# Optimization experiments

Measured on AMD Instinct MI355X. Metric: run time of the kernel, lower is better.

Reference implementation:

```python
import jax, jax.numpy as jnp
import numpy as np

N, F, U, H = 4096, 512, 64, 8
EDGE_PROB = 0.01
NEG_MASK = -10e9  # matches keras-gat masking constant
LRELU_SLOPE = 0.2


def setup_inputs() -> dict:
    key = jax.random.key(0)
    kX, kA, kI, kW, kS, kN, kB = jax.random.split(key, 7)
    X = jax.random.normal(kX, (1, N, F), dtype=jnp.float32)
    # sparse binary adjacency with self loops (layer expects preprocessed self-loops)
    A = (jax.random.uniform(kA, (N, N)) < EDGE_PROB).astype(jnp.float32)
    A = jnp.maximum(A, jnp.eye(N, dtype=jnp.float32))
    out_indices = jax.random.randint(kI, (1, 128), 0, N).astype(jnp.int64)
    scale_w = 1.0 / np.sqrt(F)
    scale_a = 1.0 / np.sqrt(U)
    W = jax.random.normal(kW, (H, F, U), dtype=jnp.float32) * scale_w
    a_self = jax.random.normal(kS, (H, U), dtype=jnp.float32) * scale_a
    a_neigh = jax.random.normal(kN, (H, U), dtype=jnp.float32) * scale_a
    bias = jax.random.normal(kB, (H, U), dtype=jnp.float32) * 0.1
    return {"X": X, "out_indices": out_indices, "A": A, "W": W,
            "a_self": a_self, "a_neigh": a_neigh, "bias": bias}


def reference(X, out_indices, A, W, a_self, a_neigh, bias):
    x = X[0]  # [N, F] (batch dim of 1)
    # per-head linear transform: [H, N, U]
    h = jnp.einsum('nf,hfu->hnu', x, W)
    # additive attention logits: f_self[i] + f_neigh[j]
    f_self = jnp.einsum('hnu,hu->hn', h, a_self)    # [H, N]
    f_neigh = jnp.einsum('hnu,hu->hn', h, a_neigh)  # [H, N]
    scores = f_self[:, :, None] + f_neigh[:, None, :]  # [H, N, N]
    scores = jax.nn.leaky_relu(scores, negative_slope=LRELU_SLOPE)
    # mask non-edges (standard, non-saliency path): dense += -10e9 * (1 - A)
    scores = scores + NEG_MASK * (1.0 - A)[None, :, :]
    attn = jax.nn.softmax(scores, axis=-1)  # [H, N, N]
    # weighted aggregation + bias
    out = jnp.einsum('hnm,hmu->hnu', attn, h) + bias[:, None, :]  # [H, N, U]
    # concat heads: [N, H*U], then activation (relu)
    out = jnp.transpose(out, (1, 0, 2)).reshape(N, H * U)
    out = jax.nn.relu(out)
    return out[None, :, :]  # [1, N, H*U]; final_layer=False -> all nodes
```

## Files before the change

### kernel.cpp

```cpp
#include <hip/hip_runtime.h>
#include <hip/hip_bf16.h>

#define N_NODES 4096
#define F_DIM   512
#define U_DIM   64
#define H_HEADS 8
#define C_DIM   512
#define LRELU_S 0.2f
#define MAXE    128
#define GEMM_BLOCKS 512

typedef __attribute__((ext_vector_type(8))) short bf16x8;
typedef __attribute__((ext_vector_type(4))) float f32x4;

__device__ inline unsigned short f2bf(float f) {
  union { float f; unsigned u; } v; v.f = f;
  unsigned r = v.u + 0x7FFFu + ((v.u >> 16) & 1u);
  return (unsigned short)(r >> 16);
}
__device__ inline float bf2f(unsigned short b) {
  union { unsigned u; float f; } v; v.u = ((unsigned)b) << 16;
  return v.f;
}

__global__ __launch_bounds__(256) void front_kernel(
    const float* __restrict__ X, const float* __restrict__ W,
    const float* __restrict__ A, const float* __restrict__ a_self,
    const float* __restrict__ a_neigh, unsigned short* __restrict__ hb,
    float* __restrict__ fsT, float* __restrict__ fnT, int* __restrict__ deg,
    unsigned short* __restrict__ nbr) {
  __shared__ unsigned short As[64][72];
  __shared__ unsigned short Bs[64][72];
  __shared__ int wsum[4];

  const int t    = threadIdx.x;
  const int lane = t & 63;
  const int w    = t >> 6;

  if ((int)blockIdx.x < GEMM_BLOCKS) {
    const int mblk = blockIdx.x & 63;
    const int head = blockIdx.x >> 6;
    const int m0   = mblk * 64;
    const float* Wh = W + (size_t)head * F_DIM * U_DIM;

    const int wr = w >> 1, wc = w & 1;
    const int arow = t >> 2;
    const int akc  = (t & 3) * 16;
    const int bu   = t & 63;
    const int bjc  = (t >> 6) * 16;

    f32x4 acc[2][2] = {};

    for (int k0 = 0; k0 < F_DIM; k0 += 64) {
      {
        const float* src = X + (size_t)(m0 + arow) * F_DIM + k0 + akc;
        float4 f0 = ((const float4*)src)[0];
        float4 f1 = ((const float4*)src)[1];
        float4 f2 = ((const float4*)src)[2];
        float4 f3 = ((const float4*)src)[3];
        bf16x8 u0 = {(short)f2bf(f0.x), (short)f2bf(f0.y), (short)f2bf(f0.z),
                     (short)f2bf(f0.w), (short)f2bf(f1.x), (short)f2bf(f1.y),
                     (short)f2bf(f1.z), (short)f2bf(f1.w)};
        bf16x8 u1 = {(short)f2bf(f2.x), (short)f2bf(f2.y), (short)f2bf(f2.z),
                     (short)f2bf(f2.w), (short)f2bf(f3.x), (short)f2bf(f3.y),
                     (short)f2bf(f3.z), (short)f2bf(f3.w)};
        *(bf16x8*)&As[arow][akc]     = u0;
        *(bf16x8*)&As[arow][akc + 8] = u1;
      }
      {
        float bv[16];
#pragma unroll
        for (int j = 0; j < 16; ++j)
          bv[j] = Wh[(size_t)(k0 + bjc + j) * U_DIM + bu];
        bf16x8 w0 = {(short)f2bf(bv[0]), (short)f2bf(bv[1]), (short)f2bf(bv[2]),
                     (short)f2bf(bv[3]), (short)f2bf(bv[4]), (short)f2bf(bv[5]),
                     (short)f2bf(bv[6]), (short)f2bf(bv[7])};
        bf16x8 w1 = {(short)f2bf(bv[8]),  (short)f2bf(bv[9]),
                     (short)f2bf(bv[10]), (short)f2bf(bv[11]),
                     (short)f2bf(bv[12]), (short)f2bf(bv[13]),
                     (short)f2bf(bv[14]), (short)f2bf(bv[15])};
        *(bf16x8*)&Bs[bu][bjc]     = w0;
        *(bf16x8*)&Bs[bu][bjc + 8] = w1;
      }
      __syncthreads();

      const int r  = lane & 15;
      const int ko = (lane >> 4) * 8;
#pragma unroll
      for (int kk = 0; kk < 2; ++kk) {
        bf16x8 af0 = *(const bf16x8*)&As[wr * 32 + r][kk * 32 + ko];
        bf16x8 af1 = *(const bf16x8*)&As[wr * 32 + 16 + r][kk * 32 + ko];
        bf16x8 bf0 = *(const bf16x8*)&Bs[wc * 32 + r][kk * 32 + ko];
        bf16x8 bf1 = *(const bf16x8*)&Bs[wc * 32 + 16 + r][kk * 32 + ko];
        acc[0][0] = __builtin_amdgcn_mfma_f32_16x16x32_bf16(af0, bf0, acc[0][0], 0, 0, 0);
        acc[0][1] = __builtin_amdgcn_mfma_f32_16x16x32_bf16(af0, bf1, acc[0][1], 0, 0, 0);
        acc[1][0] = __builtin_amdgcn_mfma_f32_16x16x32_bf16(af1, bf0, acc[1][0], 0, 0, 0);
        acc[1][1] = __builtin_amdgcn_mfma_f32_16x16x32_bf16(af1, bf1, acc[1][1], 0, 0, 0);
      }
      __syncthreads();
    }

#pragma unroll
    for (int mi = 0; mi < 2; ++mi) {
#pragma unroll
      for (int ni = 0; ni < 2; ++ni) {
        const int rb = wr * 32 + mi * 16 + (lane >> 4) * 4;
        const int cl = wc * 32 + ni * 16 + (lane & 15);
#pragma unroll
        for (int reg = 0; reg < 4; ++reg) {
          unsigned short hv = f2bf(acc[mi][ni][reg]);
          hb[(size_t)(m0 + rb + reg) * C_DIM + head * U_DIM + cl] = hv;
          As[rb + reg][cl] = hv;
        }
      }
    }
    __syncthreads();
    if (t < 128) {
      const int r = t & 63;
      const float* avec = (t >= 64) ? a_neigh + head * U_DIM
                                    : a_self + head * U_DIM;
      float s = 0.f;
#pragma unroll
      for (int u = 0; u < 64; ++u) s += bf2f(As[r][u]) * avec[u];
      float* dst = (t >= 64) ? fnT : fsT;
      dst[(size_t)(m0 + r) * H_HEADS + head] = s;
    }
  } else {
    const int i = (int)blockIdx.x - GEMM_BLOCKS;
    const float* Arow = A + (size_t)i * N_NODES;
    float av[4][4];
#pragma unroll
    for (int q = 0; q < 4; ++q) {
      float4 x = *(const float4*)(Arow + 4 * t + q * 1024);
      av[q][0] = x.x; av[q][1] = x.y; av[q][2] = x.z; av[q][3] = x.w;
    }
    int c = 0;
#pragma unroll
    for (int q = 0; q < 4; ++q)
#pragma unroll
      for (int j = 0; j < 4; ++j) c += (av[q][j] != 0.0f) ? 1 : 0;

    int psum = c;
#pragma unroll
    for (int off = 1; off < 64; off <<= 1) {
      int v = __shfl_up(psum, off);
      if (lane >= off) psum += v;
    }
    if (lane == 63) wsum[w] = psum;
    __syncthreads();
    int woff = 0;
#pragma unroll
    for (int k = 0; k < 4; ++k)
      if (k < w) woff += wsum[k];
    int E = wsum[0] + wsum[1] + wsum[2] + wsum[3];
    if (E > MAXE) E = MAXE;

    int pos = woff + psum - c;
#pragma unroll
    for (int q = 0; q < 4; ++q) {
#pragma unroll
      for (int j = 0; j < 4; ++j) {
        if (av[q][j] != 0.0f) {
          if (pos < MAXE)
            nbr[(size_t)i * MAXE + pos] = (unsigned short)(4 * t + q * 1024 + j);
          ++pos;
        }
      }
    }
    if (t == 0) deg[i] = E;
  }
}

__global__ __launch_bounds__(256) void attn_kernel(
    const unsigned short* __restrict__ hb, const float* __restrict__ fsT,
    const float* __restrict__ fnT, const float* __restrict__ bias,
    const int* __restrict__ deg, const unsigned short* __restrict__ nbr,
    float* __restrict__ out) {
  __shared__ int   eidx[4][MAXE];
  __shared__ float p[4][MAXE][9];

  const int t    = threadIdx.x;
  const int lane = t & 63;
  const int w    = t >> 6;
  const int i    = blockIdx.x * 4 + w;
  const int E    = deg[i];

  float fsv[8];
  {
    float4 a = *(const float4*)(fsT + (size_t)i * H_HEADS);
    float4 b = *(const float4*)(fsT + (size_t)i * H_HEADS + 4);
    fsv[0]=a.x; fsv[1]=a.y; fsv[2]=a.z; fsv[3]=a.w;
    fsv[4]=b.x; fsv[5]=b.y; fsv[6]=b.z; fsv[7]=b.w;
  }

  float pmax[8];
#pragma unroll
  for (int h = 0; h < 8; ++h) pmax[h] = -1e30f;
  for (int e = lane; e < E; e += 64) {
    const int j = (int)nbr[(size_t)i * MAXE + e];
    eidx[w][e] = j;
    float4 a = *(const float4*)(fnT + (size_t)j * H_HEADS);
    float4 b = *(const float4*)(fnT + (size_t)j * H_HEADS + 4);
    float fnv[8] = {a.x, a.y, a.z, a.w, b.x, b.y, b.z, b.w};
#pragma unroll
    for (int h = 0; h < 8; ++h) {
      float sc = fsv[h] + fnv[h];
      sc = (sc > 0.f) ? sc : LRELU_S * sc;
      p[w][e][h] = sc;
      pmax[h] = fmaxf(pmax[h], sc);
    }
  }
#pragma unroll
  for (int h = 0; h < 8; ++h)
#pragma unroll
    for (int off = 32; off > 0; off >>= 1)
      pmax[h] = fmaxf(pmax[h], __shfl_xor(pmax[h], off));

  float psum[8] = {};
  for (int e = lane; e < E; e += 64) {
#pragma unroll
    for (int h = 0; h < 8; ++h) {
      float ex = __expf(p[w][e][h] - pmax[h]);
      p[w][e][h] = ex;
      psum[h] += ex;
    }
  }
#pragma unroll
  for (int h = 0; h < 8; ++h)
#pragma unroll
    for (int off = 32; off > 0; off >>= 1) psum[h] += __shfl_xor(psum[h], off);

  __syncthreads();

  const int cbase = 8 * lane;
  const int hl = lane >> 3;
  float acc[8] = {};
  for (int e = 0; e < E; ++e) {
    const int j = eidx[w][e];
    uint4 v = *(const uint4*)(hb + (size_t)j * C_DIM + cbase);
    const float pe = p[w][e][hl];
    acc[0] += pe * bf2f((unsigned short)(v.x & 0xFFFFu));
    acc[1] += pe * bf2f((unsigned short)(v.x >> 16));
    acc[2] += pe * bf2f((unsigned short)(v.y & 0xFFFFu));
    acc[3] += pe * bf2f((unsigned short)(v.y >> 16));
    acc[4] += pe * bf2f((unsigned short)(v.z & 0xFFFFu));
    acc[5] += pe * bf2f((unsigned short)(v.z >> 16));
    acc[6] += pe * bf2f((unsigned short)(v.w & 0xFFFFu));
    acc[7] += pe * bf2f((unsigned short)(v.w >> 16));
  }
  float sum = psum[0];
#pragma unroll
  for (int h = 1; h < 8; ++h)
    if (hl == h) sum = psum[h];
  const float inv = 1.0f / sum;

  float4 b0 = *(const float4*)(bias + cbase);
  float4 b1 = *(const float4*)(bias + cbase + 4);
  float4 o0, o1;
  o0.x = fmaxf(acc[0] * inv + b0.x, 0.f);
  o0.y = fmaxf(acc[1] * inv + b0.y, 0.f);
  o0.z = fmaxf(acc[2] * inv + b0.z, 0.f);
  o0.w = fmaxf(acc[3] * inv + b0.w, 0.f);
  o1.x = fmaxf(acc[4] * inv + b1.x, 0.f);
  o1.y = fmaxf(acc[5] * inv + b1.y, 0.f);
  o1.z = fmaxf(acc[6] * inv + b1.z, 0.f);
  o1.w = fmaxf(acc[7] * inv + b1.w, 0.f);
  *(float4*)(out + (size_t)i * C_DIM + cbase)     = o0;
  *(float4*)(out + (size_t)i * C_DIM + cbase + 4) = o1;
}

extern "C" void kernel_launch(void* const* d_in, const int* in_sizes, int n_in,
                              void* d_out, int out_size, void* d_ws,
                              size_t ws_size, hipStream_t stream) {
  const float* X       = (const float*)d_in[0];
  const float* A       = (const float*)d_in[2];
  const float* W       = (const float*)d_in[3];
  const float* a_self  = (const float*)d_in[4];
  const float* a_neigh = (const float*)d_in[5];
  const float* bias    = (const float*)d_in[6];
  float* out = (float*)d_out;

  unsigned short* hb = (unsigned short*)d_ws;
  float* fsT = (float*)(hb + (size_t)N_NODES * C_DIM);
  float* fnT = fsT + (size_t)H_HEADS * N_NODES;
  int* deg   = (int*)(fnT + (size_t)H_HEADS * N_NODES);
  unsigned short* nbr = (unsigned short*)(deg + N_NODES);

  front_kernel<<<GEMM_BLOCKS + N_NODES, 256, 0, stream>>>(
      X, W, A, a_self, a_neigh, hb, fsT, fnT, deg, nbr);

  attn_kernel<<<N_NODES / 4, 256, 0, stream>>>(hb, fsT, fnT, bias, deg, nbr, out);
}
```

Before: 40.45 us.

## Fuse adjacency scan into per-node attention kernel and split GEMM kernel

Moves the adjacency row scan out of the combined front kernel into the attention kernel, one block per node, keeping neighbour indices in shared memory instead of writing nbr/deg to global memory. The GEMM becomes its own kernel. The aggregation now spreads 512 output columns over 256 threads with 2 columns each. This removes a global round trip for the neighbour lists, but the A read can no longer overlap the GEMM, and only one wave computes the softmax while the others wait.

```diff
diff --git a/kernel.cpp b/kernel.cpp
--- a/kernel.cpp
+++ b/kernel.cpp
@@ -23,250 +23,227 @@
   return v.f;
 }
 
-__global__ __launch_bounds__(256) void front_kernel(
+__global__ __launch_bounds__(256) void gemm_kernel(
     const float* __restrict__ X, const float* __restrict__ W,
-    const float* __restrict__ A, const float* __restrict__ a_self,
-    const float* __restrict__ a_neigh, unsigned short* __restrict__ hb,
-    float* __restrict__ fsT, float* __restrict__ fnT, int* __restrict__ deg,
-    unsigned short* __restrict__ nbr) {
+    const float* __restrict__ a_self, const float* __restrict__ a_neigh,
+    unsigned short* __restrict__ hb, float* __restrict__ fsT,
+    float* __restrict__ fnT) {
   __shared__ unsigned short As[64][72];
   __shared__ unsigned short Bs[64][72];
-  __shared__ int wsum[4];
 
   const int t    = threadIdx.x;
   const int lane = t & 63;
   const int w    = t >> 6;
 
-  if ((int)blockIdx.x < GEMM_BLOCKS) {
-    const int mblk = blockIdx.x & 63;
-    const int head = blockIdx.x >> 6;
-    const int m0   = mblk * 64;
-    const float* Wh = W + (size_t)head * F_DIM * U_DIM;
-
-    const int wr = w >> 1, wc = w & 1;
-    const int arow = t >> 2;
-    const int akc  = (t & 3) * 16;
-    const int bu   = t & 63;
-    const int bjc  = (t >> 6) * 16;
-
-    f32x4 acc[2][2] = {};
-
-    for (int k0 = 0; k0 < F_DIM; k0 += 64) {
-      {
-        const float* src = X + (size_t)(m0 + arow) * F_DIM + k0 + akc;
-        float4 f0 = ((const float4*)src)[0];
-        float4 f1 = ((const float4*)src)[1];
-        float4 f2 = ((const float4*)src)[2];
-        float4 f3 = ((const float4*)src)[3];
-        bf16x8 u0 = {(short)f2bf(f0.x), (short)f2bf(f0.y), (short)f2bf(f0.z),
-                     (short)f2bf(f0.w), (short)f2bf(f1.x), (short)f2bf(f1.y),
-                     (short)f2bf(f1.z), (short)f2bf(f1.w)};
-        bf16x8 u1 = {(short)f2bf(f2.x), (short)f2bf(f2.y), (short)f2bf(f2.z),
-                     (short)f2bf(f2.w), (short)f2bf(f3.x), (short)f2bf(f3.y),
-                     (short)f2bf(f3.z), (short)f2bf(f3.w)};
-        *(bf16x8*)&As[arow][akc]     = u0;
-        *(bf16x8*)&As[arow][akc + 8] = u1;
-      }
-      {
-        float bv[16];
-#pragma unroll
-        for (int j = 0; j < 16; ++j)
-          bv[j] = Wh[(size_t)(k0 + bjc + j) * U_DIM + bu];
-        bf16x8 w0 = {(short)f2bf(bv[0]), (short)f2bf(bv[1]), (short)f2bf(bv[2]),
-                     (short)f2bf(bv[3]), (short)f2bf(bv[4]), (short)f2bf(bv[5]),
-                     (short)f2bf(bv[6]), (short)f2bf(bv[7])};
-        bf16x8 w1 = {(short)f2bf(bv[8]),  (short)f2bf(bv[9]),
-                     (short)f2bf(bv[10]), (short)f2bf(bv[11]),
-                     (short)f2bf(bv[12]), (short)f2bf(bv[13]),
-                     (short)f2bf(bv[14]), (short)f2bf(bv[15])};
-        *(bf16x8*)&Bs[bu][bjc]     = w0;
-        *(bf16x8*)&Bs[bu][bjc + 8] = w1;
-      }
-      __syncthreads();
-
-      const int r  = lane & 15;
-      const int ko = (lane >> 4) * 8;
-#pragma unroll
-      for (int kk = 0; kk < 2; ++kk) {
-        bf16x8 af0 = *(const bf16x8*)&As[wr * 32 + r][kk * 32 + ko];
-        bf16x8 af1 = *(const bf16x8*)&As[wr * 32 + 16 + r][kk * 32 + ko];
-        bf16x8 bf0 = *(const bf16x8*)&Bs[wc * 32 + r][kk * 32 + ko];
-        bf16x8 bf1 = *(const bf16x8*)&Bs[wc * 32 + 16 + r][kk * 32 + ko];
-        acc[0][0] = __builtin_amdgcn_mfma_f32_16x16x32_bf16(af0, bf0, acc[0][0], 0, 0, 0);
-        acc[0][1] = __builtin_amdgcn_mfma_f32_16x16x32_bf16(af0, bf1, acc[0][1], 0, 0, 0);
-        acc[1][0] = __builtin_amdgcn_mfma_f32_16x16x32_bf16(af1, bf0, acc[1][0], 0, 0, 0);
-        acc[1][1] = __builtin_amdgcn_mfma_f32_16x16x32_bf16(af1, bf1, acc[1][1], 0, 0, 0);
-      }
-      __syncthreads();
-    }
-
-#pragma unroll
-    for (int mi = 0; mi < 2; ++mi) {
-#pragma unroll
-      for (int ni = 0; ni < 2; ++ni) {
-        const int rb = wr * 32 + mi * 16 + (lane >> 4) * 4;
-        const int cl = wc * 32 + ni * 16 + (lane & 15);
-#pragma unroll
-        for (int reg = 0; reg < 4; ++reg) {
-          unsigned short hv = f2bf(acc[mi][ni][reg]);
-          hb[(size_t)(m0 + rb + reg) * C_DIM + head * U_DIM + cl] = hv;
-          As[rb + reg][cl] = hv;
-        }
-      }
+  const int mblk = blockIdx.x & 63;
+  const int head = blockIdx.x >> 6;
+  const int m0   = mblk * 64;
+  const float* Wh = W + (size_t)head * F_DIM * U_DIM;
+
+  const int wr = w >> 1, wc = w & 1;
+  const int arow = t >> 2;
+  const int akc  = (t & 3) * 16;
+  const int bu   = t & 63;
+  const int bjc  = (t >> 6) * 16;
+
+  f32x4 acc[2][2] = {};
+
+  for (int k0 = 0; k0 < F_DIM; k0 += 64) {
+    {
+      const float* src = X + (size_t)(m0 + arow) * F_DIM + k0 + akc;
+      float4 f0 = ((const float4*)src)[0];
+      float4 f1 = ((const float4*)src)[1];
+      float4 f2 = ((const float4*)src)[2];
+      float4 f3 = ((const float4*)src)[3];
+      bf16x8 u0 = {(short)f2bf(f0.x), (short)f2bf(f0.y), (short)f2bf(f0.z),
+                   (short)f2bf(f0.w), (short)f2bf(f1.x), (short)f2bf(f1.y),
+                   (short)f2bf(f1.z), (short)f2bf(f1.w)};
+      bf16x8 u1 = {(short)f2bf(f2.x), (short)f2bf(f2.y), (short)f2bf(f2.z),
+                   (short)f2bf(f2.w), (short)f2bf(f3.x), (short)f2bf(f3.y),
+                   (short)f2bf(f3.z), (short)f2bf(f3.w)};
+      *(bf16x8*)&As[arow][akc]     = u0;
+      *(bf16x8*)&As[arow][akc + 8] = u1;
+    }
+    {
+      float bv[16];
+#pragma unroll
+      for (int j = 0; j < 16; ++j)
+        bv[j] = Wh[(size_t)(k0 + bjc + j) * U_DIM + bu];
+      bf16x8 w0 = {(short)f2bf(bv[0]), (short)f2bf(bv[1]), (short)f2bf(bv[2]),
+                   (short)f2bf(bv[3]), (short)f2bf(bv[4]), (short)f2bf(bv[5]),
+                   (short)f2bf(bv[6]), (short)f2bf(bv[7])};
+      bf16x8 w1 = {(short)f2bf(bv[8]),  (short)f2bf(bv[9]),
+                   (short)f2bf(bv[10]), (short)f2bf(bv[11]),
+                   (short)f2bf(bv[12]), (short)f2bf(bv[13]),
+                   (short)f2bf(bv[14]), (short)f2bf(bv[15])};
+      *(bf16x8*)&Bs[bu][bjc]     = w0;
+      *(bf16x8*)&Bs[bu][bjc + 8] = w1;
     }
     __syncthreads();
-    if (t < 128) {
-      const int r = t & 63;
-      const float* avec = (t >= 64) ? a_neigh + head * U_DIM
-                                    : a_self + head * U_DIM;
-      float s = 0.f;
-#pragma unroll
-      for (int u = 0; u < 64; ++u) s += bf2f(As[r][u]) * avec[u];
-      float* dst = (t >= 64) ? fnT : fsT;
-      dst[(size_t)(m0 + r) * H_HEADS + head] = s;
-    }
-  } else {
-    const int i = (int)blockIdx.x - GEMM_BLOCKS;
-    const float* Arow = A + (size_t)i * N_NODES;
-    float av[4][4];
-#pragma unroll
-    for (int q = 0; q < 4; ++q) {
-      float4 x = *(const float4*)(Arow + 4 * t + q * 1024);
-      av[q][0] = x.x; av[q][1] = x.y; av[q][2] = x.z; av[q][3] = x.w;
-    }
-    int c = 0;
-#pragma unroll
-    for (int q = 0; q < 4; ++q)
-#pragma unroll
-      for (int j = 0; j < 4; ++j) c += (av[q][j] != 0.0f) ? 1 : 0;
-
-    int psum = c;
-#pragma unroll
-    for (int off = 1; off < 64; off <<= 1) {
-      int v = __shfl_up(psum, off);
-      if (lane >= off) psum += v;
-    }
-    if (lane == 63) wsum[w] = psum;
+
+    const int r  = lane & 15;
+    const int ko = (lane >> 4) * 8;
+#pragma unroll
+    for (int kk = 0; kk < 2; ++kk) {
+      bf16x8 af0 = *(const bf16x8*)&As[wr * 32 + r][kk * 32 + ko];
+      bf16x8 af1 = *(const bf16x8*)&As[wr * 32 + 16 + r][kk * 32 + ko];
+      bf16x8 bf0 = *(const bf16x8*)&Bs[wc * 32 + r][kk * 32 + ko];
+      bf16x8 bf1 = *(const bf16x8*)&Bs[wc * 32 + 16 + r][kk * 32 + ko];
+      acc[0][0] = __builtin_amdgcn_mfma_f32_16x16x32_bf16(af0, bf0, acc[0][0], 0, 0, 0);
+      acc[0][1] = __builtin_amdgcn_mfma_f32_16x16x32_bf16(af0, bf1, acc[0][1], 0, 0, 0);
+      acc[1][0] = __builtin_amdgcn_mfma_f32_16x16x32_bf16(af1, bf0, acc[1][0], 0, 0, 0);
+      acc[1][1] = __builtin_amdgcn_mfma_f32_16x16x32_bf16(af1, bf1, acc[1][1], 0, 0, 0);
+    }
     __syncthreads();
-    int woff = 0;
-#pragma unroll
-    for (int k = 0; k < 4; ++k)
-      if (k < w) woff += wsum[k];
-    int E = wsum[0] + wsum[1] + wsum[2] + wsum[3];
-    if (E > MAXE) E = MAXE;
-
-    int pos = woff + psum - c;
-#pragma unroll
-    for (int q = 0; q < 4; ++q) {
-#pragma unroll
-      for (int j = 0; j < 4; ++j) {
-        if (av[q][j] != 0.0f) {
-          if (pos < MAXE)
-            nbr[(size_t)i * MAXE + pos] = (unsigned short)(4 * t + q * 1024 + j);
-          ++pos;
-        }
-      }
-    }
-    if (t == 0) deg[i] = E;
-  }
-}
-
-__global__ __launch_bounds__(256) void attn_kernel(
-    const unsigned short* __restrict__ hb, const float* __restrict__ fsT,
-    const float* __restrict__ fnT, const float* __restrict__ bias,
-    const int* __restrict__ deg, const unsigned short* __restrict__ nbr,
-    float* __restrict__ out) {
-  __shared__ int   eidx[4][MAXE];
-  __shared__ float p[4][MAXE][9];
-
+  }
+
+#pragma unroll
+  for (int mi = 0; mi < 2; ++mi) {
+#pragma unroll
+    for (int ni = 0; ni < 2; ++ni) {
+      const int rb = wr * 32 + mi * 16 + (lane >> 4) * 4;
+      const int cl = wc * 32 + ni * 16 + (lane & 15);
+#pragma unroll
+      for (int reg = 0; reg < 4; ++reg) {
+        unsigned short hv = f2bf(acc[mi][ni][reg]);
+        hb[(size_t)(m0 + rb + reg) * C_DIM + head * U_DIM + cl] = hv;
+        As[rb + reg][cl] = hv;
+      }
+    }
+  }
+  __syncthreads();
+  if (t < 128) {
+    const int r = t & 63;
+    const float* avec = (t >= 64) ? a_neigh + head * U_DIM
+                                  : a_self + head * U_DIM;
+    float s = 0.f;
+#pragma unroll
+    for (int u = 0; u < 64; ++u) s += bf2f(As[r][u]) * avec[u];
+    float* dst = (t >= 64) ? fnT : fsT;
+    dst[(size_t)(m0 + r) * H_HEADS + head] = s;
+  }
+}
+
+__global__ __launch_bounds__(256) void scan_attn_kernel(
+    const float* __restrict__ A, const unsigned short* __restrict__ hb,
+    const float* __restrict__ fsT, const float* __restrict__ fnT,
+    const float* __restrict__ bias, float* __restrict__ out) {
+  __shared__ int   eidx[MAXE];
+  __shared__ float p[H_HEADS][MAXE];
+  __shared__ float sinv[H_HEADS];
+  __shared__ int   wsum[4];
+
+  const int i    = blockIdx.x;
   const int t    = threadIdx.x;
   const int lane = t & 63;
   const int w    = t >> 6;
-  const int i    = blockIdx.x * 4 + w;
-  const int E    = deg[i];
-
-  float fsv[8];
-  {
-    float4 a = *(const float4*)(fsT + (size_t)i * H_HEADS);
-    float4 b = *(const float4*)(fsT + (size_t)i * H_HEADS + 4);
-    fsv[0]=a.x; fsv[1]=a.y; fsv[2]=a.z; fsv[3]=a.w;
-    fsv[4]=b.x; fsv[5]=b.y; fsv[6]=b.z; fsv[7]=b.w;
-  }
-
-  float pmax[8];
-#pragma unroll
-  for (int h = 0; h < 8; ++h) pmax[h] = -1e30f;
-  for (int e = lane; e < E; e += 64) {
-    const int j = (int)nbr[(size_t)i * MAXE + e];
-    eidx[w][e] = j;
-    float4 a = *(const float4*)(fnT + (size_t)j * H_HEADS);
-    float4 b = *(const float4*)(fnT + (size_t)j * H_HEADS + 4);
-    float fnv[8] = {a.x, a.y, a.z, a.w, b.x, b.y, b.z, b.w};
+  const float* Arow = A + (size_t)i * N_NODES;
+
+  float av[4][4];
+#pragma unroll
+  for (int q = 0; q < 4; ++q) {
+    float4 x = *(const float4*)(Arow + 4 * t + q * 1024);
+    av[q][0] = x.x; av[q][1] = x.y; av[q][2] = x.z; av[q][3] = x.w;
+  }
+  int c = 0;
+#pragma unroll
+  for (int q = 0; q < 4; ++q)
+#pragma unroll
+    for (int j = 0; j < 4; ++j) c += (av[q][j] != 0.0f) ? 1 : 0;
+
+  int psum = c;
+#pragma unroll
+  for (int off = 1; off < 64; off <<= 1) {
+    int v = __shfl_up(psum, off);
+    if (lane >= off) psum += v;
+  }
+  if (lane == 63) wsum[w] = psum;
+  __syncthreads();
+  int woff = 0;
+#pragma unroll
+  for (int k = 0; k < 4; ++k)
+    if (k < w) woff += wsum[k];
+  int E = wsum[0] + wsum[1] + wsum[2] + wsum[3];
+  if (E > MAXE) E = MAXE;
+
+  int pos = woff + psum - c;
+#pragma unroll
+  for (int q = 0; q < 4; ++q) {
+#pragma unroll
+    for (int j = 0; j < 4; ++j) {
+      if (av[q][j] != 0.0f) {
+        if (pos < MAXE) eidx[pos] = 4 * t + q * 1024 + j;
+        ++pos;
+      }
+    }
+  }
+  __syncthreads();
+
+  if (w == 0) {
+    float fsv[8];
+    {
+      float4 a = *(const float4*)(fsT + (size_t)i * H_HEADS);
+      float4 b = *(const float4*)(fsT + (size_t)i * H_HEADS + 4);
+      fsv[0]=a.x; fsv[1]=a.y; fsv[2]=a.z; fsv[3]=a.w;
+      fsv[4]=b.x; fsv[5]=b.y; fsv[6]=b.z; fsv[7]=b.w;
+    }
+    float pmax[8];
+#pragma unroll
+    for (int h = 0; h < 8; ++h) pmax[h] = -1e30f;
+    for (int e = lane; e < E; e += 64) {
+      const int j = eidx[e];
+      float4 a = *(const float4*)(fnT + (size_t)j * H_HEADS);
+      float4 b = *(const float4*)(fnT + (size_t)j * H_HEADS + 4);
+      float fnv[8] = {a.x, a.y, a.z, a.w, b.x, b.y, b.z, b.w};
+#pragma unroll
+      for (int h = 0; h < 8; ++h) {
+        float sc = fsv[h] + fnv[h];
+        sc = (sc > 0.f) ? sc : LRELU_S * sc;
+        p[h][e] = sc;
+        pmax[h] = fmaxf(pmax[h], sc);
+      }
+    }
+#pragma unroll
+    for (int h = 0; h < 8; ++h)
+#pragma unroll
+      for (int off = 32; off > 0; off >>= 1)
+        pmax[h] = fmaxf(pmax[h], __shfl_xor(pmax[h], off));
+
+    float psm[8] = {};
+    for (int e = lane; e < E; e += 64) {
+#pragma unroll
+      for (int h = 0; h < 8; ++h) {
+        float ex = __expf(p[h][e] - pmax[h]);
+        p[h][e] = ex;
+        psm[h] += ex;
+      }
+    }
 #pragma unroll
     for (int h = 0; h < 8; ++h) {
-      float sc = fsv[h] + fnv[h];
-      sc = (sc > 0.f) ? sc : LRELU_S * sc;
-      p[w][e][h] = sc;
-      pmax[h] = fmaxf(pmax[h], sc);
-    }
-  }
-#pragma unroll
-  for (int h = 0; h < 8; ++h)
-#pragma unroll
-    for (int off = 32; off > 0; off >>= 1)
-      pmax[h] = fmaxf(pmax[h], __shfl_xor(pmax[h], off));
-
-  float psum[8] = {};
-  for (int e = lane; e < E; e += 64) {
-#pragma unroll
-    for (int h = 0; h < 8; ++h) {
-      float ex = __expf(p[w][e][h] - pmax[h]);
-      p[w][e][h] = ex;
-      psum[h] += ex;
-    }
-  }
-#pragma unroll
-  for (int h = 0; h < 8; ++h)
-#pragma unroll
-    for (int off = 32; off > 0; off >>= 1) psum[h] += __shfl_xor(psum[h], off);
-
-  __syncthreads();
-
-  const int cbase = 8 * lane;
-  const int hl = lane >> 3;
-  float acc[8] = {};
+#pragma unroll
+      for (int off = 32; off > 0; off >>= 1) psm[h] += __shfl_xor(psm[h], off);
+      if (lane == 0) sinv[h] = 1.0f / psm[h];
+    }
+  }
+  __syncthreads();
+
+  const int c0 = 2 * t;
+  const int hl = t >> 5;
+  const float* ph = p[hl];
+  float a0 = 0.f, a1 = 0.f;
+#pragma unroll 4
   for (int e = 0; e < E; ++e) {
-    const int j = eidx[w][e];
-    uint4 v = *(const uint4*)(hb + (size_t)j * C_DIM + cbase);
-    const float pe = p[w][e][hl];
-    acc[0] += pe * bf2f((unsigned short)(v.x & 0xFFFFu));
-    acc[1] += pe * bf2f((unsigned short)(v.x >> 16));
-    acc[2] += pe * bf2f((unsigned short)(v.y & 0xFFFFu));
-    acc[3] += pe * bf2f((unsigned short)(v.y >> 16));
-    acc[4] += pe * bf2f((unsigned short)(v.z & 0xFFFFu));
-    acc[5] += pe * bf2f((unsigned short)(v.z >> 16));
-    acc[6] += pe * bf2f((unsigned short)(v.w & 0xFFFFu));
-    acc[7] += pe * bf2f((unsigned short)(v.w >> 16));
-  }
-  float sum = psum[0];
-#pragma unroll
-  for (int h = 1; h < 8; ++h)
-    if (hl == h) sum = psum[h];
-  const float inv = 1.0f / sum;
-
-  float4 b0 = *(const float4*)(bias + cbase);
-  float4 b1 = *(const float4*)(bias + cbase + 4);
-  float4 o0, o1;
-  o0.x = fmaxf(acc[0] * inv + b0.x, 0.f);
-  o0.y = fmaxf(acc[1] * inv + b0.y, 0.f);
-  o0.z = fmaxf(acc[2] * inv + b0.z, 0.f);
-  o0.w = fmaxf(acc[3] * inv + b0.w, 0.f);
-  o1.x = fmaxf(acc[4] * inv + b1.x, 0.f);
-  o1.y = fmaxf(acc[5] * inv + b1.y, 0.f);
-  o1.z = fmaxf(acc[6] * inv + b1.z, 0.f);
-  o1.w = fmaxf(acc[7] * inv + b1.w, 0.f);
-  *(float4*)(out + (size_t)i * C_DIM + cbase)     = o0;
-  *(float4*)(out + (size_t)i * C_DIM + cbase + 4) = o1;
+    unsigned v = *(const unsigned*)(hb + (size_t)eidx[e] * C_DIM + c0);
+    const float pe = ph[e];
+    a0 += pe * bf2f((unsigned short)(v & 0xFFFFu));
+    a1 += pe * bf2f((unsigned short)(v >> 16));
+  }
+  const float inv = sinv[hl];
+  float2 bv = *(const float2*)(bias + c0);
+  float2 o;
+  o.x = fmaxf(a0 * inv + bv.x, 0.f);
+  o.y = fmaxf(a1 * inv + bv.y, 0.f);
+  *(float2*)(out + (size_t)i * C_DIM + c0) = o;
 }
 
 extern "C" void kernel_launch(void* const* d_in, const int* in_sizes, int n_in,
@@ -283,11 +260,9 @@
   unsigned short* hb = (unsigned short*)d_ws;
   float* fsT = (float*)(hb + (size_t)N_NODES * C_DIM);
   float* fnT = fsT + (size_t)H_HEADS * N_NODES;
-  int* deg   = (int*)(fnT + (size_t)H_HEADS * N_NODES);
-  unsigned short* nbr = (unsigned short*)(deg + N_NODES);
-
-  front_kernel<<<GEMM_BLOCKS + N_NODES, 256, 0, stream>>>(
-      X, W, A, a_self, a_neigh, hb, fsT, fnT, deg, nbr);
-
-  attn_kernel<<<N_NODES / 4, 256, 0, stream>>>(hb, fsT, fnT, bias, deg, nbr, out);
-}
+
+  gemm_kernel<<<GEMM_BLOCKS, 256, 0, stream>>>(X, W, a_self, a_neigh, hb,
+                                               fsT, fnT);
+
+  scan_attn_kernel<<<N_NODES, 256, 0, stream>>>(A, hb, fsT, fnT, bias, out);
+}
```

Measured after the change: 49.38 us. +22.1%, slower.

## Scan adjacency rows per wavefront instead of per block

Applied to the files above, without the earlier changes.

The adjacency compaction now gives each 64-lane wavefront a whole row (two rows per wave, eight per block) instead of one row per 256-thread block. This cuts the scan grid from 4096 blocks to 512, drops the shared-memory cross-wave sum and the __syncthreads, and takes the row total from a lane shuffle. In exchange each thread keeps 16 float4 loads live in registers, which raises register pressure and may lower occupancy of the shared front kernel.

```diff
diff --git a/kernel.cpp b/kernel.cpp
--- a/kernel.cpp
+++ b/kernel.cpp
@@ -9,6 +9,8 @@
 #define LRELU_S 0.2f
 #define MAXE    128
 #define GEMM_BLOCKS 512
+#define SCAN_BLOCKS 512
+#define ROWS_PER_WAVE 2
 
 typedef __attribute__((ext_vector_type(8))) short bf16x8;
 typedef __attribute__((ext_vector_type(4))) float f32x4;
@@ -31,7 +33,6 @@
     unsigned short* __restrict__ nbr) {
   __shared__ unsigned short As[64][72];
   __shared__ unsigned short Bs[64][72];
-  __shared__ int wsum[4];
 
   const int t    = threadIdx.x;
   const int lane = t & 63;
@@ -126,48 +127,43 @@
       dst[(size_t)(m0 + r) * H_HEADS + head] = s;
     }
   } else {
-    const int i = (int)blockIdx.x - GEMM_BLOCKS;
-    const float* Arow = A + (size_t)i * N_NODES;
-    float av[4][4];
-#pragma unroll
-    for (int q = 0; q < 4; ++q) {
-      float4 x = *(const float4*)(Arow + 4 * t + q * 1024);
-      av[q][0] = x.x; av[q][1] = x.y; av[q][2] = x.z; av[q][3] = x.w;
-    }
-    int c = 0;
-#pragma unroll
-    for (int q = 0; q < 4; ++q)
-#pragma unroll
-      for (int j = 0; j < 4; ++j) c += (av[q][j] != 0.0f) ? 1 : 0;
-
-    int psum = c;
-#pragma unroll
-    for (int off = 1; off < 64; off <<= 1) {
-      int v = __shfl_up(psum, off);
-      if (lane >= off) psum += v;
-    }
-    if (lane == 63) wsum[w] = psum;
-    __syncthreads();
-    int woff = 0;
-#pragma unroll
-    for (int k = 0; k < 4; ++k)
-      if (k < w) woff += wsum[k];
-    int E = wsum[0] + wsum[1] + wsum[2] + wsum[3];
-    if (E > MAXE) E = MAXE;
-
-    int pos = woff + psum - c;
-#pragma unroll
-    for (int q = 0; q < 4; ++q) {
-#pragma unroll
-      for (int j = 0; j < 4; ++j) {
-        if (av[q][j] != 0.0f) {
-          if (pos < MAXE)
-            nbr[(size_t)i * MAXE + pos] = (unsigned short)(4 * t + q * 1024 + j);
-          ++pos;
-        }
-      }
-    }
-    if (t == 0) deg[i] = E;
+    const int sb = (int)blockIdx.x - GEMM_BLOCKS;
+#pragma unroll
+    for (int rr = 0; rr < ROWS_PER_WAVE; ++rr) {
+      const int i = (sb * 4 + w) * ROWS_PER_WAVE + rr;
+      const float* Arow = A + (size_t)i * N_NODES;
+      float4 buf[16];
+#pragma unroll
+      for (int q = 0; q < 16; ++q)
+        buf[q] = *(const float4*)(Arow + q * 256 + 4 * lane);
+
+      int c = 0;
+#pragma unroll
+      for (int q = 0; q < 16; ++q) {
+        c += (buf[q].x != 0.f) ? 1 : 0;
+        c += (buf[q].y != 0.f) ? 1 : 0;
+        c += (buf[q].z != 0.f) ? 1 : 0;
+        c += (buf[q].w != 0.f) ? 1 : 0;
+      }
+      int psum = c;
+#pragma unroll
+      for (int off = 1; off < 64; off <<= 1) {
+        int v = __shfl_up(psum, off);
+        if (lane >= off) psum += v;
+      }
+      const int E = __shfl(psum, 63);
+      int pos = psum - c;
+      unsigned short* nrow = nbr + (size_t)i * MAXE;
+#pragma unroll
+      for (int q = 0; q < 16; ++q) {
+        const int gb = q * 256 + 4 * lane;
+        if (buf[q].x != 0.f) { if (pos < MAXE) nrow[pos] = (unsigned short)(gb);     ++pos; }
+        if (buf[q].y != 0.f) { if (pos < MAXE) nrow[pos] = (unsigned short)(gb + 1); ++pos; }
+        if (buf[q].z != 0.f) { if (pos < MAXE) nrow[pos] = (unsigned short)(gb + 2); ++pos; }
+        if (buf[q].w != 0.f) { if (pos < MAXE) nrow[pos] = (unsigned short)(gb + 3); ++pos; }
+      }
+      if (lane == 63) deg[i] = (E > MAXE) ? MAXE : E;
+    }
   }
 }
 
@@ -286,8 +282,9 @@
   int* deg   = (int*)(fnT + (size_t)H_HEADS * N_NODES);
   unsigned short* nbr = (unsigned short*)(deg + N_NODES);
 
-  front_kernel<<<GEMM_BLOCKS + N_NODES, 256, 0, stream>>>(
+  front_kernel<<<GEMM_BLOCKS + SCAN_BLOCKS, 256, 0, stream>>>(
       X, W, A, a_self, a_neigh, hb, fsT, fnT, deg, nbr);
 
-  attn_kernel<<<N_NODES / 4, 256, 0, stream>>>(hb, fsT, fnT, bias, deg, nbr, out);
-}
+  attn_kernel<<<N_NODES / 4, 256, 0, stream>>>(hb, fsT, fnT, bias, deg, nbr,
+                                               out);
+}
```

Result: slower. 43.86 us (+8.4%).
